# Kernel tuning notes

Measured on AMD Instinct MI355X. Metric: run time of the kernel, lower is better.

Reference implementation:

```python
import jax, jax.numpy as jnp
import numpy as np

LN_EPS = 1e-5
BOUNDARY_ID = 0  # boundary_ids = {space_id} = {0}


def setup_inputs() -> dict:
    key = jax.random.key(0)
    k1, k2, k3 = jax.random.split(key, 3)
    B, T, D = 16, 8192, 256
    x = jax.random.normal(k1, (B, T, D), dtype=jnp.float32)
    input_ids = jax.random.randint(k2, (B, T), 0, 8, dtype=jnp.int64)
    W_proj = jax.random.normal(k3, (D, D), dtype=jnp.float32) / np.sqrt(D)
    b_proj = jnp.zeros((D,), dtype=jnp.float32)
    gamma = jnp.ones((D,), dtype=jnp.float32)
    beta = jnp.zeros((D,), dtype=jnp.float32)
    return {"x": x, "input_ids": input_ids, "W_proj": W_proj,
            "b_proj": b_proj, "gamma": gamma, "beta": beta}


def _pool(x, input_ids):
    # Boundary-defined segment mean pooling, vectorized via segment_sum.
    B, T, D = x.shape
    boundary = input_ids == BOUNDARY_ID                       # [B,T]
    nonb = ~boundary
    # A segment starts at a non-boundary token at t=0 or right after a boundary.
    prev_is_b = jnp.concatenate(
        [jnp.ones((B, 1), dtype=bool), boundary[:, :-1]], axis=1)
    start = nonb & prev_is_b
    seg = jnp.cumsum(start.astype(jnp.int32), axis=1) - 1     # seg idx per token
    MAXW = T  # static upper bound on number of segments (jit-safe padding)
    row_off = jnp.arange(B, dtype=jnp.int32)[:, None] * MAXW
    dump = B * MAXW  # boundary tokens go to a dummy segment, dropped below
    flat_ids = jnp.where(nonb, seg + row_off, dump).reshape(-1)
    sums = jax.ops.segment_sum(x.reshape(-1, D), flat_ids,
                               num_segments=B * MAXW + 1)[:-1]
    counts = jax.ops.segment_sum(jnp.ones((B * T,), x.dtype), flat_ids,
                                 num_segments=B * MAXW + 1)[:-1]
    sums = sums.reshape(B, MAXW, D)
    counts = counts.reshape(B, MAXW)
    mask = (counts > 0).astype(x.dtype)                       # [B,MAXW]
    padded = sums / jnp.maximum(counts, 1.0)[..., None]       # zeros where empty
    return padded, mask


def reference(x, input_ids, W_proj, b_proj, gamma, beta):
    padded, mask = _pool(x, input_ids)
    out = jnp.einsum('bwd,ed->bwe', padded, W_proj) + b_proj  # nn.Linear
    mu = jnp.mean(out, axis=-1, keepdims=True)
    var = jnp.mean(jnp.square(out - mu), axis=-1, keepdims=True)
    out = (out - mu) * jax.lax.rsqrt(var + LN_EPS) * gamma + beta
    return out, mask
```

## Files before the change

kernel.cpp:

```cpp
#include <hip/hip_runtime.h>
#include <hip/hip_bf16.h>
#include <math.h>

#define BB 16
#define TT 8192
#define DD 256
#define MAXSEG 4096
#define RPB 16
#define LN_EPS 1e-5f

__device__ inline float4 f4add(float4 a, float4 b) {
    a.x += b.x; a.y += b.y; a.z += b.z; a.w += b.w; return a;
}

__global__ __launch_bounds__(256) void prelude(const float* __restrict__ W,
                                               const float* __restrict__ bp,
                                               const float* __restrict__ gamma,
                                               const float* __restrict__ beta,
                                               float* __restrict__ Wt,
                                               float* __restrict__ ln_empty) {
    __shared__ float s1[256];
    __shared__ float s2[256];
    int e = threadIdx.x;
    if (blockIdx.x < DD) {
        int d = blockIdx.x;
        Wt[d * DD + e] = W[e * DD + d];
        return;
    }
    float v = bp[e];
    s1[e] = v;
    s2[e] = v * v;
    __syncthreads();
    for (int o = 128; o > 0; o >>= 1) {
        if (e < o) { s1[e] += s1[e + o]; s2[e] += s2[e + o]; }
        __syncthreads();
    }
    float mu = s1[0] / (float)DD;
    float var = s2[0] / (float)DD - mu * mu;
    float rs = rsqrtf(fmaxf(var, 0.f) + LN_EPS);
    ln_empty[e] = (v - mu) * rs * gamma[e] + beta[e];
}

__global__ __launch_bounds__(1024) void seg_scan(const int* __restrict__ ids,
                                                 int* __restrict__ counts,
                                                 int* __restrict__ seg_start,
                                                 int* __restrict__ nseg_g,
                                                 float* __restrict__ mask_out) {
    const int TPT = 8;
    __shared__ int wtot_s[16];
    __shared__ int wtot_n[16];
    __shared__ int segs[MAXSEG];
    __shared__ int pvals[MAXSEG];

    int b = blockIdx.x;
    int tid = threadIdx.x;
    int lane = tid & 63;
    int wv = tid >> 6;
    const int* row = ids + b * TT;
    int t0 = tid * TPT;

    int4 q0 = ((const int4*)(row + t0))[0];
    int4 q1 = ((const int4*)(row + t0))[1];
    int v[TPT] = {q0.x, q0.y, q0.z, q0.w, q1.x, q1.y, q1.z, q1.w};
    int prev = (tid == 0) ? 0 : row[t0 - 1];

    bool nb[TPT], st[TPT];
    int cstart = 0, cnon = 0;
#pragma unroll
    for (int j = 0; j < TPT; ++j) {
        nb[j] = (v[j] != 0);
        int pv = (j == 0) ? prev : v[j - 1];
        st[j] = nb[j] && (pv == 0);
        cstart += st[j] ? 1 : 0;
        cnon += nb[j] ? 1 : 0;
    }

    int ss = cstart, sn = cnon;
#pragma unroll
    for (int o = 1; o < 64; o <<= 1) {
        int us = __shfl_up(ss, o);
        int un = __shfl_up(sn, o);
        if (lane >= o) { ss += us; sn += un; }
    }
    if (lane == 63) { wtot_s[wv] = ss; wtot_n[wv] = sn; }
    __syncthreads();

    int bs = 0, bn = 0, tot_s = 0, tot_n = 0;
#pragma unroll
    for (int j = 0; j < 16; ++j) {
        int a = wtot_s[j], c = wtot_n[j];
        if (j < wv) { bs += a; bn += c; }
        tot_s += a; tot_n += c;
    }
    bs += ss - cstart;
    bn += sn - cnon;

#pragma unroll
    for (int j = 0; j < TPT; ++j) {
        if (st[j]) { segs[bs] = t0 + j; pvals[bs] = bn; bs++; }
        bn += nb[j] ? 1 : 0;
    }
    __syncthreads();

    int ns = tot_s;
    for (int w = tid; w < TT; w += 1024) {
        int c = 0;
        if (w < ns) {
            int pe = (w + 1 < ns) ? pvals[w + 1] : tot_n;
            c = pe - pvals[w];
            seg_start[b * TT + w] = segs[w];
        }
        counts[b * TT + w] = c;
        mask_out[b * TT + w] = (w < ns) ? 1.0f : 0.0f;
    }
    if (tid == 0) nseg_g[b] = ns;
}

__global__ __launch_bounds__(256) void pool_gemm_ln(
    const float* __restrict__ x, const float* __restrict__ Wt,
    const float* __restrict__ bp, const float* __restrict__ gamma,
    const float* __restrict__ beta, const int* __restrict__ counts,
    const int* __restrict__ seg_start, const int* __restrict__ nseg,
    const float* __restrict__ ln_e, float* __restrict__ out) {
    __shared__ float pooled[RPB][DD];

    int b = blockIdx.x;
    int wbase = blockIdx.y * RPB;
    int ns = nseg[b];
    int tid = threadIdx.x;
    int lane = tid & 63;
    int wv = tid >> 6;
    int r0 = wv * 4;
    size_t outbase = ((size_t)(b * TT + wbase)) * DD + 4 * lane;

    if (wbase >= ns) {
        float4 lv = *(const float4*)(ln_e + 4 * lane);
#pragma unroll
        for (int r = 0; r < 4; ++r)
            *(float4*)(out + outbase + (size_t)(r0 + r) * DD) = lv;
        return;
    }
    int nr = min(RPB, ns - wbase);

#pragma unroll
    for (int r = 0; r < 4; ++r) {
        int row = r0 + r;
        if (row < nr) {
            int w = wbase + row;
            int s = seg_start[b * TT + w];
            int len = counts[b * TT + w];
            const float4* xp = (const float4*)(x + ((size_t)(b * TT + s)) * DD) + lane;
            float4 a0 = {0, 0, 0, 0}, a1 = a0, a2 = a0, a3 = a0;
            int t = 0;
            for (; t + 4 <= len; t += 4) {
                a0 = f4add(a0, xp[(t + 0) * 64]);
                a1 = f4add(a1, xp[(t + 1) * 64]);
                a2 = f4add(a2, xp[(t + 2) * 64]);
                a3 = f4add(a3, xp[(t + 3) * 64]);
            }
            for (; t < len; ++t) a0 = f4add(a0, xp[t * 64]);
            a0 = f4add(f4add(a0, a1), f4add(a2, a3));
            float inv = 1.f / (float)len;
            a0.x *= inv; a0.y *= inv; a0.z *= inv; a0.w *= inv;
            *(float4*)&pooled[row][lane * 4] = a0;
        }
    }

    float4 acc[4];
    float4 bias4 = *(const float4*)(bp + 4 * lane);
#pragma unroll
    for (int r = 0; r < 4; ++r) acc[r] = bias4;

    if (r0 < nr) {
        const float4* WtR = (const float4*)Wt;
#pragma unroll 2
        for (int d0 = 0; d0 < DD; d0 += 4) {
            float4 w0 = WtR[(d0 + 0) * 64 + lane];
            float4 w1 = WtR[(d0 + 1) * 64 + lane];
            float4 w2 = WtR[(d0 + 2) * 64 + lane];
            float4 w3 = WtR[(d0 + 3) * 64 + lane];
#pragma unroll
            for (int r = 0; r < 4; ++r) {
                const float4 p = *(const float4*)&pooled[r0 + r][d0];
                acc[r].x = fmaf(p.x, w0.x, acc[r].x);
                acc[r].y = fmaf(p.x, w0.y, acc[r].y);
                acc[r].z = fmaf(p.x, w0.z, acc[r].z);
                acc[r].w = fmaf(p.x, w0.w, acc[r].w);
                acc[r].x = fmaf(p.y, w1.x, acc[r].x);
                acc[r].y = fmaf(p.y, w1.y, acc[r].y);
                acc[r].z = fmaf(p.y, w1.z, acc[r].z);
                acc[r].w = fmaf(p.y, w1.w, acc[r].w);
                acc[r].x = fmaf(p.z, w2.x, acc[r].x);
                acc[r].y = fmaf(p.z, w2.y, acc[r].y);
                acc[r].z = fmaf(p.z, w2.z, acc[r].z);
                acc[r].w = fmaf(p.z, w2.w, acc[r].w);
                acc[r].x = fmaf(p.w, w3.x, acc[r].x);
                acc[r].y = fmaf(p.w, w3.y, acc[r].y);
                acc[r].z = fmaf(p.w, w3.z, acc[r].z);
                acc[r].w = fmaf(p.w, w3.w, acc[r].w);
            }
        }
    }

    float4 ga4 = *(const float4*)(gamma + 4 * lane);
    float4 be4 = *(const float4*)(beta + 4 * lane);
    float4 lv = *(const float4*)(ln_e + 4 * lane);
#pragma unroll
    for (int r = 0; r < 4; ++r) {
        int row = r0 + r;
        float4 v;
        if (row < nr) {
            float s = acc[r].x + acc[r].y + acc[r].z + acc[r].w;
            float sq = acc[r].x * acc[r].x + acc[r].y * acc[r].y +
                       acc[r].z * acc[r].z + acc[r].w * acc[r].w;
#pragma unroll
            for (int o = 32; o > 0; o >>= 1) {
                s += __shfl_down(s, o);
                sq += __shfl_down(sq, o);
            }
            s = __shfl(s, 0);
            sq = __shfl(sq, 0);
            float mu = s * (1.f / (float)DD);
            float var = sq * (1.f / (float)DD) - mu * mu;
            float rs = rsqrtf(fmaxf(var, 0.f) + LN_EPS);
            v.x = (acc[r].x - mu) * rs * ga4.x + be4.x;
            v.y = (acc[r].y - mu) * rs * ga4.y + be4.y;
            v.z = (acc[r].z - mu) * rs * ga4.z + be4.z;
            v.w = (acc[r].w - mu) * rs * ga4.w + be4.w;
        } else {
            v = lv;
        }
        *(float4*)(out + outbase + (size_t)row * DD) = v;
    }
}

extern "C" void kernel_launch(void* const* d_in, const int* in_sizes, int n_in,
                              void* d_out, int out_size, void* d_ws, size_t ws_size,
                              hipStream_t stream) {
    const float* x = (const float*)d_in[0];
    const int* ids = (const int*)d_in[1];
    const float* W = (const float*)d_in[2];
    const float* bp = (const float*)d_in[3];
    const float* gamma = (const float*)d_in[4];
    const float* beta = (const float*)d_in[5];

    float* out = (float*)d_out;
    float* mask = out + (size_t)BB * TT * DD;

    char* ws = (char*)d_ws;
    int* counts = (int*)ws;
    int* seg_start = (int*)(ws + (size_t)BB * TT * 4);
    int* nseg = (int*)(ws + (size_t)2 * BB * TT * 4);
    float* Wt = (float*)(ws + (size_t)2 * BB * TT * 4 + 256);
    float* ln_e = Wt + DD * DD;

    hipLaunchKernelGGL(prelude, dim3(DD + 1), dim3(DD), 0, stream,
                       W, bp, gamma, beta, Wt, ln_e);
    hipLaunchKernelGGL(seg_scan, dim3(BB), dim3(1024), 0, stream,
                       ids, counts, seg_start, nseg, mask);
    hipLaunchKernelGGL(pool_gemm_ln, dim3(BB, TT / RPB), dim3(256), 0, stream,
                       x, Wt, bp, gamma, beta, counts, seg_start, nseg, ln_e, out);
}
```

Baseline: 285.9 us.

## Merge setup kernels and restructure pooled GEMM to column-split with 8-row blocks

Merges the weight-transpose/empty-LN prelude into the segment-scan kernel so one launch does all setup. The pooling GEMM now uses 128-thread blocks over 8 rows. Each thread owns two output columns for all rows and reuses each loaded weight pair across every row, with the next weights prefetched. LayerNorm statistics are reduced through shared memory across two waves, which adds a block barrier and halves rows per block, doubling the grid.

```diff
diff --git a/kernel.cpp b/kernel.cpp
--- a/kernel.cpp
+++ b/kernel.cpp
@@ -6,56 +6,64 @@
 #define TT 8192
 #define DD 256
 #define MAXSEG 4096
-#define RPB 16
+#define RPB 8
 #define LN_EPS 1e-5f
 
 __device__ inline float4 f4add(float4 a, float4 b) {
     a.x += b.x; a.y += b.y; a.z += b.z; a.w += b.w; return a;
 }
 
-__global__ __launch_bounds__(256) void prelude(const float* __restrict__ W,
-                                               const float* __restrict__ bp,
-                                               const float* __restrict__ gamma,
-                                               const float* __restrict__ beta,
-                                               float* __restrict__ Wt,
-                                               float* __restrict__ ln_empty) {
-    __shared__ float s1[256];
-    __shared__ float s2[256];
-    int e = threadIdx.x;
-    if (blockIdx.x < DD) {
-        int d = blockIdx.x;
-        Wt[d * DD + e] = W[e * DD + d];
-        return;
-    }
-    float v = bp[e];
-    s1[e] = v;
-    s2[e] = v * v;
-    __syncthreads();
-    for (int o = 128; o > 0; o >>= 1) {
-        if (e < o) { s1[e] += s1[e + o]; s2[e] += s2[e + o]; }
-        __syncthreads();
-    }
-    float mu = s1[0] / (float)DD;
-    float var = s2[0] / (float)DD - mu * mu;
-    float rs = rsqrtf(fmaxf(var, 0.f) + LN_EPS);
-    ln_empty[e] = (v - mu) * rs * gamma[e] + beta[e];
-}
-
-__global__ __launch_bounds__(1024) void seg_scan(const int* __restrict__ ids,
-                                                 int* __restrict__ counts,
-                                                 int* __restrict__ seg_start,
-                                                 int* __restrict__ nseg_g,
-                                                 float* __restrict__ mask_out) {
-    const int TPT = 8;
+__global__ __launch_bounds__(1024) void setup_kernel(
+    const int* __restrict__ ids, const float* __restrict__ W,
+    const float* __restrict__ bp, const float* __restrict__ gamma,
+    const float* __restrict__ beta, int* __restrict__ counts,
+    int* __restrict__ seg_start, int* __restrict__ nseg_g,
+    float* __restrict__ mask_out, float* __restrict__ Wt,
+    float* __restrict__ ln_empty) {
     __shared__ int wtot_s[16];
     __shared__ int wtot_n[16];
     __shared__ int segs[MAXSEG];
     __shared__ int pvals[MAXSEG];
 
-    int b = blockIdx.x;
     int tid = threadIdx.x;
     int lane = tid & 63;
     int wv = tid >> 6;
+
+    if (blockIdx.x >= BB) {
+        int bi = blockIdx.x - BB;
+        if (bi < 64) {
+            int d = bi * 4 + (tid >> 8);
+            int e = tid & 255;
+            Wt[d * DD + e] = W[e * DD + d];
+        } else if (wv == 0) {
+            int e0 = lane * 4;
+            float4 v = *(const float4*)(bp + e0);
+            float s = v.x + v.y + v.z + v.w;
+            float sq = v.x * v.x + v.y * v.y + v.z * v.z + v.w * v.w;
+#pragma unroll
+            for (int o = 32; o > 0; o >>= 1) {
+                s += __shfl_down(s, o);
+                sq += __shfl_down(sq, o);
+            }
+            s = __shfl(s, 0);
+            sq = __shfl(sq, 0);
+            float mu = s * (1.f / (float)DD);
+            float var = sq * (1.f / (float)DD) - mu * mu;
+            float rs = rsqrtf(fmaxf(var, 0.f) + LN_EPS);
+            float4 ge = *(const float4*)(gamma + e0);
+            float4 be = *(const float4*)(beta + e0);
+            float4 o4;
+            o4.x = (v.x - mu) * rs * ge.x + be.x;
+            o4.y = (v.y - mu) * rs * ge.y + be.y;
+            o4.z = (v.z - mu) * rs * ge.z + be.z;
+            o4.w = (v.w - mu) * rs * ge.w + be.w;
+            *(float4*)(ln_empty + e0) = o4;
+        }
+        return;
+    }
+
+    const int TPT = 8;
+    int b = blockIdx.x;
     const int* row = ids + b * TT;
     int t0 = tid * TPT;
 
@@ -116,13 +124,14 @@
     if (tid == 0) nseg_g[b] = ns;
 }
 
-__global__ __launch_bounds__(256) void pool_gemm_ln(
+__global__ __launch_bounds__(128) void pool_gemm_ln(
     const float* __restrict__ x, const float* __restrict__ Wt,
     const float* __restrict__ bp, const float* __restrict__ gamma,
     const float* __restrict__ beta, const int* __restrict__ counts,
     const int* __restrict__ seg_start, const int* __restrict__ nseg,
     const float* __restrict__ ln_e, float* __restrict__ out) {
     __shared__ float pooled[RPB][DD];
+    __shared__ float red[2][RPB][2];
 
     int b = blockIdx.x;
     int wbase = blockIdx.y * RPB;
@@ -130,27 +139,28 @@
     int tid = threadIdx.x;
     int lane = tid & 63;
     int wv = tid >> 6;
-    int r0 = wv * 4;
-    size_t outbase = ((size_t)(b * TT + wbase)) * DD + 4 * lane;
+    size_t rowbase = ((size_t)(b * TT + wbase)) * DD;
 
     if (wbase >= ns) {
         float4 lv = *(const float4*)(ln_e + 4 * lane);
+        float* o = out + rowbase + (size_t)(wv * 4) * DD + 4 * lane;
 #pragma unroll
         for (int r = 0; r < 4; ++r)
-            *(float4*)(out + outbase + (size_t)(r0 + r) * DD) = lv;
+            *(float4*)(o + (size_t)r * DD) = lv;
         return;
     }
     int nr = min(RPB, ns - wbase);
 
 #pragma unroll
     for (int r = 0; r < 4; ++r) {
-        int row = r0 + r;
+        int row = wv * 4 + r;
+        float4 a0 = {0, 0, 0, 0};
         if (row < nr) {
             int w = wbase + row;
             int s = seg_start[b * TT + w];
             int len = counts[b * TT + w];
             const float4* xp = (const float4*)(x + ((size_t)(b * TT + s)) * DD) + lane;
-            float4 a0 = {0, 0, 0, 0}, a1 = a0, a2 = a0, a3 = a0;
+            float4 a1 = a0, a2 = a0, a3 = a0;
             int t = 0;
             for (; t + 4 <= len; t += 4) {
                 a0 = f4add(a0, xp[(t + 0) * 64]);
@@ -162,75 +172,70 @@
             a0 = f4add(f4add(a0, a1), f4add(a2, a3));
             float inv = 1.f / (float)len;
             a0.x *= inv; a0.y *= inv; a0.z *= inv; a0.w *= inv;
-            *(float4*)&pooled[row][lane * 4] = a0;
-        }
-    }
-
-    float4 acc[4];
-    float4 bias4 = *(const float4*)(bp + 4 * lane);
-#pragma unroll
-    for (int r = 0; r < 4; ++r) acc[r] = bias4;
-
-    if (r0 < nr) {
-        const float4* WtR = (const float4*)Wt;
-#pragma unroll 2
-        for (int d0 = 0; d0 < DD; d0 += 4) {
-            float4 w0 = WtR[(d0 + 0) * 64 + lane];
-            float4 w1 = WtR[(d0 + 1) * 64 + lane];
-            float4 w2 = WtR[(d0 + 2) * 64 + lane];
-            float4 w3 = WtR[(d0 + 3) * 64 + lane];
-#pragma unroll
-            for (int r = 0; r < 4; ++r) {
-                const float4 p = *(const float4*)&pooled[r0 + r][d0];
-                acc[r].x = fmaf(p.x, w0.x, acc[r].x);
-                acc[r].y = fmaf(p.x, w0.y, acc[r].y);
-                acc[r].z = fmaf(p.x, w0.z, acc[r].z);
-                acc[r].w = fmaf(p.x, w0.w, acc[r].w);
-                acc[r].x = fmaf(p.y, w1.x, acc[r].x);
-                acc[r].y = fmaf(p.y, w1.y, acc[r].y);
-                acc[r].z = fmaf(p.y, w1.z, acc[r].z);
-                acc[r].w = fmaf(p.y, w1.w, acc[r].w);
-                acc[r].x = fmaf(p.z, w2.x, acc[r].x);
-                acc[r].y = fmaf(p.z, w2.y, acc[r].y);
-                acc[r].z = fmaf(p.z, w2.z, acc[r].z);
-                acc[r].w = fmaf(p.z, w2.w, acc[r].w);
-                acc[r].x = fmaf(p.w, w3.x, acc[r].x);
-                acc[r].y = fmaf(p.w, w3.y, acc[r].y);
-                acc[r].z = fmaf(p.w, w3.z, acc[r].z);
-                acc[r].w = fmaf(p.w, w3.w, acc[r].w);
-            }
-        }
-    }
-
-    float4 ga4 = *(const float4*)(gamma + 4 * lane);
-    float4 be4 = *(const float4*)(beta + 4 * lane);
-    float4 lv = *(const float4*)(ln_e + 4 * lane);
-#pragma unroll
-    for (int r = 0; r < 4; ++r) {
-        int row = r0 + r;
-        float4 v;
-        if (row < nr) {
-            float s = acc[r].x + acc[r].y + acc[r].z + acc[r].w;
-            float sq = acc[r].x * acc[r].x + acc[r].y * acc[r].y +
-                       acc[r].z * acc[r].z + acc[r].w * acc[r].w;
-#pragma unroll
-            for (int o = 32; o > 0; o >>= 1) {
-                s += __shfl_down(s, o);
-                sq += __shfl_down(sq, o);
-            }
-            s = __shfl(s, 0);
-            sq = __shfl(sq, 0);
-            float mu = s * (1.f / (float)DD);
-            float var = sq * (1.f / (float)DD) - mu * mu;
-            float rs = rsqrtf(fmaxf(var, 0.f) + LN_EPS);
-            v.x = (acc[r].x - mu) * rs * ga4.x + be4.x;
-            v.y = (acc[r].y - mu) * rs * ga4.y + be4.y;
-            v.z = (acc[r].z - mu) * rs * ga4.z + be4.z;
-            v.w = (acc[r].w - mu) * rs * ga4.w + be4.w;
-        } else {
-            v = lv;
-        }
-        *(float4*)(out + outbase + (size_t)row * DD) = v;
+        }
+        *(float4*)&pooled[row][lane * 4] = a0;
+    }
+    __syncthreads();
+
+    int c0 = wv * 128 + lane * 2;
+    float2 acc[RPB];
+    float2 bias2 = *(const float2*)(bp + c0);
+#pragma unroll
+    for (int r = 0; r < RPB; ++r) acc[r] = bias2;
+
+    const float* Wc = Wt + c0;
+    float2 w0 = *(const float2*)(Wc + 0 * DD);
+    float2 w1 = *(const float2*)(Wc + 1 * DD);
+    float2 w2 = *(const float2*)(Wc + 2 * DD);
+    float2 w3 = *(const float2*)(Wc + 3 * DD);
+#pragma unroll 1
+    for (int d0 = 0; d0 < DD; d0 += 4) {
+        int dn = (d0 + 4) & 255;
+        float2 n0 = *(const float2*)(Wc + (dn + 0) * DD);
+        float2 n1 = *(const float2*)(Wc + (dn + 1) * DD);
+        float2 n2 = *(const float2*)(Wc + (dn + 2) * DD);
+        float2 n3 = *(const float2*)(Wc + (dn + 3) * DD);
+#pragma unroll
+        for (int r = 0; r < RPB; ++r) {
+            const float4 p = *(const float4*)&pooled[r][d0];
+            acc[r].x = fmaf(p.x, w0.x, acc[r].x);
+            acc[r].y = fmaf(p.x, w0.y, acc[r].y);
+            acc[r].x = fmaf(p.y, w1.x, acc[r].x);
+            acc[r].y = fmaf(p.y, w1.y, acc[r].y);
+            acc[r].x = fmaf(p.z, w2.x, acc[r].x);
+            acc[r].y = fmaf(p.z, w2.y, acc[r].y);
+            acc[r].x = fmaf(p.w, w3.x, acc[r].x);
+            acc[r].y = fmaf(p.w, w3.y, acc[r].y);
+        }
+        w0 = n0; w1 = n1; w2 = n2; w3 = n3;
+    }
+
+#pragma unroll
+    for (int r = 0; r < RPB; ++r) {
+        float s = acc[r].x + acc[r].y;
+        float sq = acc[r].x * acc[r].x + acc[r].y * acc[r].y;
+#pragma unroll
+        for (int o = 32; o > 0; o >>= 1) {
+            s += __shfl_down(s, o);
+            sq += __shfl_down(sq, o);
+        }
+        if (lane == 0) { red[wv][r][0] = s; red[wv][r][1] = sq; }
+    }
+    __syncthreads();
+
+    float ga0 = gamma[c0], ga1 = gamma[c0 + 1];
+    float be0 = beta[c0], be1 = beta[c0 + 1];
+#pragma unroll
+    for (int r = 0; r < RPB; ++r) {
+        float s = red[0][r][0] + red[1][r][0];
+        float sq = red[0][r][1] + red[1][r][1];
+        float mu = s * (1.f / (float)DD);
+        float var = sq * (1.f / (float)DD) - mu * mu;
+        float rs = rsqrtf(fmaxf(var, 0.f) + LN_EPS);
+        float2 v;
+        v.x = (acc[r].x - mu) * rs * ga0 + be0;
+        v.y = (acc[r].y - mu) * rs * ga1 + be1;
+        *(float2*)(out + rowbase + (size_t)r * DD + c0) = v;
     }
 }
 
@@ -254,10 +259,9 @@
     float* Wt = (float*)(ws + (size_t)2 * BB * TT * 4 + 256);
     float* ln_e = Wt + DD * DD;
 
-    hipLaunchKernelGGL(prelude, dim3(DD + 1), dim3(DD), 0, stream,
-                       W, bp, gamma, beta, Wt, ln_e);
-    hipLaunchKernelGGL(seg_scan, dim3(BB), dim3(1024), 0, stream,
-                       ids, counts, seg_start, nseg, mask);
-    hipLaunchKernelGGL(pool_gemm_ln, dim3(BB, TT / RPB), dim3(256), 0, stream,
+    hipLaunchKernelGGL(setup_kernel, dim3(BB + 64 + 1), dim3(1024), 0, stream,
+                       ids, W, bp, gamma, beta, counts, seg_start, nseg, mask,
+                       Wt, ln_e);
+    hipLaunchKernelGGL(pool_gemm_ln, dim3(BB, TT / RPB), dim3(128), 0, stream,
                        x, Wt, bp, gamma, beta, counts, seg_start, nseg, ln_e, out);
 }
```

Result: no change. 281.3 us (-1.6%).
